# Optimization experiments

Hardware: AMD Instinct MI355X
Metric: run time of the kernel (lower is better)

## Reference

```python
import jax, jax.numpy as jnp
import numpy as np

N = 20000
E = 320000
H = 4
IN_DIM = 2000
# (in_dim, per-head out channels, concat) for each GATConv layer
LAYER_DIMS = [(2000, 128, True), (512, 64, True), (256, 32, True), (128, 64, False)]
NEG_SLOPE = 0.2  # PyG GATConv LeakyReLU slope


def setup_inputs() -> dict:
    key = jax.random.key(0)
    ks = jax.random.split(key, 2 + 4 * len(LAYER_DIMS))
    inp = {
        "x": jax.random.normal(ks[0], (N, IN_DIM), dtype=jnp.float32),
        "edge_index": jax.random.randint(ks[1], (2, E), 0, N, dtype=jnp.int64),
    }
    for i, (din, c, concat) in enumerate(LAYER_DIMS):
        k0, k1, k2, _ = jax.random.split(ks[2 + i], 4)
        inp[f"W{i}"] = (jax.random.normal(k0, (din, H * c), dtype=jnp.float32)
                         * (1.0 / np.sqrt(din)).astype(np.float32))
        inp[f"as{i}"] = jax.random.normal(k1, (H, c), dtype=jnp.float32) * 0.1
        inp[f"ad{i}"] = jax.random.normal(k2, (H, c), dtype=jnp.float32) * 0.1
        inp[f"b{i}"] = jnp.zeros((H * c if concat else c,), dtype=jnp.float32)
    return inp


def gat_conv(x, src, dst, W, att_src, att_dst, bias, concat):
    n, c = x.shape[0], W.shape[1] // H
    h = (x @ W).reshape(n, H, c)                      # (N,H,C) per-head features
    a_s = jnp.einsum("nhc,hc->nh", h, att_src)        # (N,H) source logits
    a_d = jnp.einsum("nhc,hc->nh", h, att_dst)        # (N,H) target logits
    e = a_s[src] + a_d[dst]                           # (E,H) per-edge logits
    e = jnp.where(e > 0, e, NEG_SLOPE * e)            # leaky_relu
    # segment softmax over edges sharing the same target node
    m = jax.ops.segment_max(e, dst, num_segments=n)   # (N,H)
    ex = jnp.exp(e - m[dst])
    denom = jax.ops.segment_sum(ex, dst, num_segments=n)
    alpha = ex / denom[dst]                           # (E,H)
    # weighted scatter-aggregate of source features
    out = jax.ops.segment_sum(alpha[:, :, None] * h[src], dst, num_segments=n)  # (N,H,C)
    out = out.reshape(n, H * c) if concat else out.mean(axis=1)
    return out + bias


def reference(x, edge_index, W0, as0, ad0, b0, W1, as1, ad1, b1,
              W2, as2, ad2, b2, W3, as3, ad3, b3):
    loops = jnp.arange(N, dtype=edge_index.dtype)
    src = jnp.concatenate([edge_index[0], loops])     # add self-loops (PyG default)
    dst = jnp.concatenate([edge_index[1], loops])
    params = [(W0, as0, ad0, b0), (W1, as1, ad1, b1), (W2, as2, ad2, b2), (W3, as3, ad3, b3)]
    h = x
    for i, (W, a_s, a_d, b) in enumerate(params):
        concat = LAYER_DIMS[i][2]
        h = gat_conv(h, src, dst, W, a_s, a_d, b, concat)
        if i < len(params) - 1:
            h = jax.nn.elu(h)  # dropout inactive in eval mode
    return h
```

## Files before the change

kernel.cpp:

```cpp
#include <hip/hip_runtime.h>
#include <hip/hip_bf16.h>

#define GN 20000
#define GE 320000
#define GETOT (GE + GN)
#define GH 4
#define NROW 20096

typedef __attribute__((ext_vector_type(8))) _Float16 f16x8;
typedef __attribute__((ext_vector_type(4))) float f32x4;

__global__ void detect_dtype_kernel(const void* __restrict__ ei, int* __restrict__ flag) {
    if (threadIdx.x == 0 && blockIdx.x == 0) {
        const long long* p = (const long long*)ei;
        int ok = 1;
        for (int i = 0; i < 16; ++i) {
            long long v = p[i];
            if (v < 0 || v >= GN) ok = 0;
        }
        *flag = ok;
    }
}

__device__ __forceinline__ int load_idx(const void* ei, int is64, long long pos) {
    if (is64) return (int)((const long long*)ei)[pos];
    return ((const int*)ei)[pos];
}

__global__ void hist_kernel(const void* __restrict__ ei, const int* __restrict__ flagp,
                            int* __restrict__ counts) {
    int e = blockIdx.x * blockDim.x + threadIdx.x;
    if (e >= GETOT) return;
    int d;
    if (e < GE) d = load_idx(ei, *flagp, (long long)GE + e);
    else        d = e - GE;
    atomicAdd(&counts[d], 1);
}

__global__ __launch_bounds__(1024) void scan_kernel(const int* __restrict__ counts,
                                                    int* __restrict__ offsets,
                                                    int* __restrict__ cursor) {
    __shared__ int sh[1024];
    const int tid = threadIdx.x;
    constexpr int CH = 20;
    const int base = tid * CH;
    int loc[CH];
    int sum = 0;
#pragma unroll
    for (int i = 0; i < CH; ++i) {
        int idx = base + i;
        int v = (idx < GN) ? counts[idx] : 0;
        loc[i] = sum;
        sum += v;
    }
    sh[tid] = sum;
    __syncthreads();
    for (int o = 1; o < 1024; o <<= 1) {
        int t = (tid >= o) ? sh[tid - o] : 0;
        __syncthreads();
        sh[tid] += t;
        __syncthreads();
    }
    const int excl = tid ? sh[tid - 1] : 0;
#pragma unroll
    for (int i = 0; i < CH; ++i) {
        int idx = base + i;
        if (idx < GN) {
            int o = excl + loc[i];
            offsets[idx] = o;
            cursor[idx]  = o;
        }
    }
    if (tid == 1023) offsets[GN] = sh[1023];
}

__global__ void scatter_kernel(const void* __restrict__ ei, const int* __restrict__ flagp,
                               int* __restrict__ cursor, int* __restrict__ csr_src) {
    int e = blockIdx.x * blockDim.x + threadIdx.x;
    if (e >= GETOT) return;
    int s, d;
    if (e < GE) {
        int is64 = *flagp;
        s = load_idx(ei, is64, e);
        d = load_idx(ei, is64, (long long)GE + e);
    } else {
        s = d = e - GE;
    }
    int pos = atomicAdd(&cursor[d], 1);
    csr_src[pos] = s;
}

__device__ __forceinline__ float h2f(unsigned u) {
    unsigned short us = (unsigned short)u;
    _Float16 h;
    __builtin_memcpy(&h, &us, 2);
    return (float)h;
}
__device__ __forceinline__ unsigned short f2h_bits(float v) {
    _Float16 h = (_Float16)v;
    unsigned short us;
    __builtin_memcpy(&us, &h, 2);
    return us;
}

__global__ __launch_bounds__(256) void convert_xf16(const float* __restrict__ x,
                                                    unsigned* __restrict__ xf) {
    const int CPR = 2016 / 8;
    long long idx = (long long)blockIdx.x * 256 + threadIdx.x;
    if (idx >= (long long)NROW * CPR) return;
    int row = (int)(idx / CPR);
    int col = (int)(idx % CPR) * 8;
    uint4 hp = make_uint4(0, 0, 0, 0);
    if (row < GN && col < 2000) {
        const float* p = x + (size_t)row * 2000 + col;
        float4 v0 = *(const float4*)p, v1 = *(const float4*)(p + 4);
        hp.x = (unsigned)f2h_bits(v0.x) | ((unsigned)f2h_bits(v0.y) << 16);
        hp.y = (unsigned)f2h_bits(v0.z) | ((unsigned)f2h_bits(v0.w) << 16);
        hp.z = (unsigned)f2h_bits(v1.x) | ((unsigned)f2h_bits(v1.y) << 16);
        hp.w = (unsigned)f2h_bits(v1.z) | ((unsigned)f2h_bits(v1.w) << 16);
    }
    *(uint4*)(xf + (((size_t)row * 2016 + col) >> 1)) = hp;
}

__global__ void convert_wt(const float* __restrict__ W,
                           _Float16* __restrict__ thi,
                           int K, int N, int Kpad) {
    __shared__ float tile[32][33];
    int kb = blockIdx.x * 32, nb = blockIdx.y * 32;
    for (int i = threadIdx.y; i < 32; i += 8) {
        int k = kb + i, n = nb + threadIdx.x;
        tile[i][threadIdx.x] = (k < K) ? W[(size_t)k * N + n] : 0.f;
    }
    __syncthreads();
    for (int i = threadIdx.y; i < 32; i += 8) {
        int n = nb + i, k = kb + threadIdx.x;
        thi[(size_t)n * Kpad + k] = (_Float16)tile[threadIdx.x][i];
    }
}

__device__ __forceinline__ int swz(int a) { return a ^ (((a >> 6) & 7) << 4); }
__device__ __forceinline__ int invswz(int p) {
    int b8 = (p >> 8) & 1, b7 = (p >> 7) & 1;
    int a6 = ((p >> 6) & 1) ^ b8;
    int a5 = ((p >> 5) & 1) ^ b7;
    int a4 = ((p >> 4) & 1) ^ a6;
    return (p & ~0x70) | (a4 << 4) | (a5 << 5) | (a6 << 6);
}

#define GLDS16(gsrc, ldst) __builtin_amdgcn_global_load_lds( \
    (const __attribute__((address_space(1))) void*)(gsrc),   \
    (__attribute__((address_space(3))) void*)(ldst), 16, 0, 0)

template <int MODE>
__global__ __launch_bounds__(256, 4) void gemm_f16(
        const _Float16* __restrict__ Af, int lda,
        const _Float16* __restrict__ Whi,
        int Kpad, void* __restrict__ Cp, int M, int N, int NC) {
    __shared__ char lds[32768];
    const int tid = threadIdx.x;

    const int nwg = gridDim.x;
    const int q = nwg >> 3, r = nwg & 7;
    const int xcd = blockIdx.x & 7, sub = blockIdx.x >> 3;
    const int orig = (xcd < r ? xcd * (q + 1) : r * (q + 1) + (xcd - r) * q) + sub;
    const int brow = (orig / NC) * 128;
    const int bcol = (orig % NC) * 128;

    const int lane = tid & 63, wid = tid >> 6;
    const int wr = wid >> 1, wc = wid & 1;
    const int l4 = lane & 15, kg = lane >> 4;

    int row8[2], ecol[2];
#pragma unroll
    for (int p = 0; p < 2; ++p) {
        int a = invswz(p * 4096 + tid * 16);
        row8[p] = a >> 6;
        ecol[p] = (a & 63) >> 1;
    }
    int rA[2], rB[2];
#pragma unroll
    for (int p = 0; p < 2; ++p) {
        rA[p] = brow + row8[p];
        rB[p] = bcol + row8[p];
    }

    auto STAGE = [&](int buf, int k0) {
        char* bb = lds + buf * 16384;
#pragma unroll
        for (int p = 0; p < 2; ++p) {
            GLDS16(Af  + (size_t)rA[p] * lda  + k0 + ecol[p], bb + p * 4096 + tid * 16);
            GLDS16(Whi + (size_t)rB[p] * Kpad + k0 + ecol[p], bb + 8192 + p * 4096 + tid * 16);
        }
    };

    int aoff[4], boff[4];
#pragma unroll
    for (int m = 0; m < 4; ++m) {
        aoff[m] = swz((wr * 64 + m * 16 + l4) * 64 + kg * 16);
        boff[m] = swz((wc * 64 + m * 16 + l4) * 64 + kg * 16);
    }

    f32x4 acc[4][4];
#pragma unroll
    for (int m = 0; m < 4; ++m)
#pragma unroll
        for (int n = 0; n < 4; ++n) acc[m][n] = (f32x4)(0.f);

    const int nk = Kpad / 32;
    STAGE(0, 0);

    for (int t = 0; t < nk; ++t) {
        if (t + 1 < nk) {
            STAGE((t + 1) & 1, (t + 1) * 32);
            asm volatile("s_waitcnt vmcnt(4)" ::: "memory");
        } else {
            asm volatile("s_waitcnt vmcnt(0)" ::: "memory");
        }
        __builtin_amdgcn_s_barrier();
        __builtin_amdgcn_sched_barrier(0);

        char* bb = lds + (t & 1) * 16384;
        f16x8 av[4], wh[4];
#pragma unroll
        for (int m = 0; m < 4; ++m) av[m] = *(const f16x8*)(bb + aoff[m]);
#pragma unroll
        for (int n = 0; n < 4; ++n) wh[n] = *(const f16x8*)(bb + 8192 + boff[n]);
        asm volatile("s_waitcnt lgkmcnt(0)" ::: "memory");
        __builtin_amdgcn_sched_barrier(0);

#pragma unroll
        for (int m = 0; m < 4; ++m)
#pragma unroll
            for (int n = 0; n < 4; ++n)
                acc[m][n] = __builtin_amdgcn_mfma_f32_16x16x32_f16(av[m], wh[n], acc[m][n], 0, 0, 0);
        __builtin_amdgcn_s_barrier();
    }

#pragma unroll
    for (int m = 0; m < 4; ++m) {
        int gr0 = brow + wr * 64 + m * 16 + (lane >> 4) * 4;
#pragma unroll
        for (int n = 0; n < 4; ++n) {
            int gc = bcol + wc * 64 + n * 16 + l4;
#pragma unroll
            for (int rr2 = 0; rr2 < 4; ++rr2) {
                int gr = gr0 + rr2;
                if (gr < M) {
                    size_t o = (size_t)gr * N + gc;
                    float v = acc[m][n][rr2];
                    if constexpr (MODE == 2) ((float*)Cp)[o] = v;
                    else                     ((_Float16*)Cp)[o] = (_Float16)v;
                }
            }
        }
    }
}

template <bool F16>
__global__ void att_sd_kernel(const void* __restrict__ hfeat,
                              const float* __restrict__ att_s,
                              const float* __restrict__ att_d,
                              float* __restrict__ a_s, float* __restrict__ a_d,
                              int C) {
    int wid  = (blockIdx.x * blockDim.x + threadIdx.x) >> 6;
    int lane = threadIdx.x & 63;
    if (wid >= GN) return;
#pragma unroll
    for (int h = 0; h < GH; ++h) {
        float ss = 0.f, sd = 0.f;
        for (int cc = lane; cc < C; cc += 64) {
            size_t idx = (size_t)wid * GH * C + h * C + cc;
            float v = F16 ? h2f(((const unsigned short*)hfeat)[idx])
                          : ((const float*)hfeat)[idx];
            ss += v * att_s[h * C + cc];
            sd += v * att_d[h * C + cc];
        }
#pragma unroll
        for (int o = 32; o; o >>= 1) {
            ss += __shfl_xor(ss, o);
            sd += __shfl_xor(sd, o);
        }
        if (lane == 0) { a_s[wid * GH + h] = ss; a_d[wid * GH + h] = sd; }
    }
}

template <int C, int CPT, int BLOCK>
__global__ __launch_bounds__(BLOCK) void gat_aggregate_f16(
        const unsigned short* __restrict__ hfeat,
        const float* __restrict__ a_s,
        const float* __restrict__ a_d,
        const int* __restrict__ offsets,
        const int* __restrict__ csr_src,
        const float* __restrict__ bias,
        unsigned short* __restrict__ of16) {
    constexpr int HC = GH * C;
    static_assert(BLOCK * CPT == HC, "coverage");
    const int n     = blockIdx.x;
    const int tid   = threadIdx.x;
    const int start = offsets[n];
    const int end   = offsets[n + 1];

    __shared__ float s_m[GH];
    __shared__ float s_den[GH];
    __shared__ int   s_src[64];
    __shared__ float s_al[GH][68];

    const float4 ad4 = *(const float4*)(a_d + n * GH);
    const float adh[GH] = {ad4.x, ad4.y, ad4.z, ad4.w};

    if (tid < 64) {
        float lmax[GH], lsum[GH];
#pragma unroll
        for (int h = 0; h < GH; ++h) lmax[h] = -1e30f;
        for (int e = start + tid; e < end; e += 64) {
            int s = csr_src[e];
            float4 as4 = *(const float4*)(a_s + s * GH);
            float l[GH] = {as4.x + adh[0], as4.y + adh[1], as4.z + adh[2], as4.w + adh[3]};
#pragma unroll
            for (int h = 0; h < GH; ++h) {
                float ll = l[h] > 0.f ? l[h] : 0.2f * l[h];
                lmax[h] = fmaxf(lmax[h], ll);
            }
        }
#pragma unroll
        for (int h = 0; h < GH; ++h)
#pragma unroll
            for (int o = 32; o; o >>= 1) lmax[h] = fmaxf(lmax[h], __shfl_xor(lmax[h], o));
#pragma unroll
        for (int h = 0; h < GH; ++h) lsum[h] = 0.f;
        for (int e = start + tid; e < end; e += 64) {
            int s = csr_src[e];
            float4 as4 = *(const float4*)(a_s + s * GH);
            float l[GH] = {as4.x + adh[0], as4.y + adh[1], as4.z + adh[2], as4.w + adh[3]};
#pragma unroll
            for (int h = 0; h < GH; ++h) {
                float ll = l[h] > 0.f ? l[h] : 0.2f * l[h];
                lsum[h] += __expf(ll - lmax[h]);
            }
        }
#pragma unroll
        for (int h = 0; h < GH; ++h)
#pragma unroll
            for (int o = 32; o; o >>= 1) lsum[h] += __shfl_xor(lsum[h], o);
        if (tid == 0) {
#pragma unroll
            for (int h = 0; h < GH; ++h) { s_m[h] = lmax[h]; s_den[h] = lsum[h]; }
        }
    }
    __syncthreads();

    float mm[GH], inv[GH];
#pragma unroll
    for (int h = 0; h < GH; ++h) { mm[h] = s_m[h]; inv[h] = 1.0f / s_den[h]; }

    const int ch0 = tid * CPT;
    const int hd  = ch0 / C;
    float acc[CPT];
#pragma unroll
    for (int j = 0; j < CPT; ++j) acc[j] = 0.f;

    for (int e0 = start; e0 < end; e0 += 64) {
        __syncthreads();
        if (tid < 64) {
            bool vld = (e0 + tid) < end;
            int s = vld ? csr_src[e0 + tid] : n;
            s_src[tid] = s;
            float4 as4 = *(const float4*)(a_s + s * GH);
            float l[GH] = {as4.x + adh[0], as4.y + adh[1], as4.z + adh[2], as4.w + adh[3]};
#pragma unroll
            for (int h = 0; h < GH; ++h) {
                float ll = l[h] > 0.f ? l[h] : 0.2f * l[h];
                s_al[h][tid] = vld ? __expf(ll - mm[h]) * inv[h] : 0.f;
            }
        }
        __syncthreads();
        int cnt = end - e0; if (cnt > 64) cnt = 64;
        int cnt4 = (cnt + 3) & ~3;
        for (int i = 0; i < cnt4; i += 4) {
            int4   ss = *(const int4*)&s_src[i];
            float4 aa = *(const float4*)&s_al[hd][i];
            if constexpr (CPT == 4) {
                uint2 v0 = ((const uint2*)(hfeat + (size_t)ss.x * HC))[tid];
                uint2 v1 = ((const uint2*)(hfeat + (size_t)ss.y * HC))[tid];
                uint2 v2 = ((const uint2*)(hfeat + (size_t)ss.z * HC))[tid];
                uint2 v3 = ((const uint2*)(hfeat + (size_t)ss.w * HC))[tid];
                acc[0] = fmaf(aa.x, h2f(v0.x & 0xffff), acc[0]);
                acc[1] = fmaf(aa.x, h2f(v0.x >> 16),    acc[1]);
                acc[2] = fmaf(aa.x, h2f(v0.y & 0xffff), acc[2]);
                acc[3] = fmaf(aa.x, h2f(v0.y >> 16),    acc[3]);
                acc[0] = fmaf(aa.y, h2f(v1.x & 0xffff), acc[0]);
                acc[1] = fmaf(aa.y, h2f(v1.x >> 16),    acc[1]);
                acc[2] = fmaf(aa.y, h2f(v1.y & 0xffff), acc[2]);
                acc[3] = fmaf(aa.y, h2f(v1.y >> 16),    acc[3]);
                acc[0] = fmaf(aa.z, h2f(v2.x & 0xffff), acc[0]);
                acc[1] = fmaf(aa.z, h2f(v2.x >> 16),    acc[1]);
                acc[2] = fmaf(aa.z, h2f(v2.y & 0xffff), acc[2]);
                acc[3] = fmaf(aa.z, h2f(v2.y >> 16),    acc[3]);
                acc[0] = fmaf(aa.w, h2f(v3.x & 0xffff), acc[0]);
                acc[1] = fmaf(aa.w, h2f(v3.x >> 16),    acc[1]);
                acc[2] = fmaf(aa.w, h2f(v3.y & 0xffff), acc[2]);
                acc[3] = fmaf(aa.w, h2f(v3.y >> 16),    acc[3]);
            } else {
                unsigned v0 = ((const unsigned*)(hfeat + (size_t)ss.x * HC))[tid];
                unsigned v1 = ((const unsigned*)(hfeat + (size_t)ss.y * HC))[tid];
                unsigned v2 = ((const unsigned*)(hfeat + (size_t)ss.z * HC))[tid];
                unsigned v3 = ((const unsigned*)(hfeat + (size_t)ss.w * HC))[tid];
                acc[0] = fmaf(aa.x, h2f(v0 & 0xffff), acc[0]);
                acc[1] = fmaf(aa.x, h2f(v0 >> 16),    acc[1]);
                acc[0] = fmaf(aa.y, h2f(v1 & 0xffff), acc[0]);
                acc[1] = fmaf(aa.y, h2f(v1 >> 16),    acc[1]);
                acc[0] = fmaf(aa.z, h2f(v2 & 0xffff), acc[0]);
                acc[1] = fmaf(aa.z, h2f(v2 >> 16),    acc[1]);
                acc[0] = fmaf(aa.w, h2f(v3 & 0xffff), acc[0]);
                acc[1] = fmaf(aa.w, h2f(v3 >> 16),    acc[1]);
            }
        }
    }

    unsigned short hs[CPT];
#pragma unroll
    for (int j = 0; j < CPT; ++j) {
        float v = acc[j] + bias[ch0 + j];
        v = v > 0.f ? v : expm1f(v);
        hs[j] = f2h_bits(v);
    }
    unsigned short* op = of16 + (size_t)n * HC + ch0;
    if constexpr (CPT == 4) {
        uint2 hw = make_uint2((unsigned)hs[0] | ((unsigned)hs[1] << 16),
                              (unsigned)hs[2] | ((unsigned)hs[3] << 16));
        *(uint2*)op = hw;
    } else {
        *(unsigned*)op = (unsigned)hs[0] | ((unsigned)hs[1] << 16);
    }
}

__global__ __launch_bounds__(128) void gat_aggregate_final(
        const float* __restrict__ hfeat,
        const float* __restrict__ a_s,
        const float* __restrict__ a_d,
        const int* __restrict__ offsets,
        const int* __restrict__ csr_src,
        const float* __restrict__ bias,
        float* __restrict__ outf) {
    constexpr int C = 64, HC = GH * C;
    const int n     = blockIdx.x;
    const int tid   = threadIdx.x;
    const int start = offsets[n];
    const int end   = offsets[n + 1];

    __shared__ float s_m[GH];
    __shared__ float s_den[GH];
    __shared__ int   s_src[64];
    __shared__ float s_al[GH][68];
    __shared__ float sacc[256];

    const float4 ad4 = *(const float4*)(a_d + n * GH);
    const float adh[GH] = {ad4.x, ad4.y, ad4.z, ad4.w};

    if (tid < 64) {
        float lmax[GH], lsum[GH];
#pragma unroll
        for (int h = 0; h < GH; ++h) lmax[h] = -1e30f;
        for (int e = start + tid; e < end; e += 64) {
            int s = csr_src[e];
            float4 as4 = *(const float4*)(a_s + s * GH);
            float l[GH] = {as4.x + adh[0], as4.y + adh[1], as4.z + adh[2], as4.w + adh[3]};
#pragma unroll
            for (int h = 0; h < GH; ++h) {
                float ll = l[h] > 0.f ? l[h] : 0.2f * l[h];
                lmax[h] = fmaxf(lmax[h], ll);
            }
        }
#pragma unroll
        for (int h = 0; h < GH; ++h)
#pragma unroll
            for (int o = 32; o; o >>= 1) lmax[h] = fmaxf(lmax[h], __shfl_xor(lmax[h], o));
#pragma unroll
        for (int h = 0; h < GH; ++h) lsum[h] = 0.f;
        for (int e = start + tid; e < end; e += 64) {
            int s = csr_src[e];
            float4 as4 = *(const float4*)(a_s + s * GH);
            float l[GH] = {as4.x + adh[0], as4.y + adh[1], as4.z + adh[2], as4.w + adh[3]};
#pragma unroll
            for (int h = 0; h < GH; ++h) {
                float ll = l[h] > 0.f ? l[h] : 0.2f * l[h];
                lsum[h] += __expf(ll - lmax[h]);
            }
        }
#pragma unroll
        for (int h = 0; h < GH; ++h)
#pragma unroll
            for (int o = 32; o; o >>= 1) lsum[h] += __shfl_xor(lsum[h], o);
        if (tid == 0) {
#pragma unroll
            for (int h = 0; h < GH; ++h) { s_m[h] = lmax[h]; s_den[h] = lsum[h]; }
        }
    }
    __syncthreads();

    float mm[GH], inv[GH];
#pragma unroll
    for (int h = 0; h < GH; ++h) { mm[h] = s_m[h]; inv[h] = 1.0f / s_den[h]; }

    const int hd = (2 * tid) / C;
    float2 acc = make_float2(0.f, 0.f);

    for (int e0 = start; e0 < end; e0 += 64) {
        __syncthreads();
        if (tid < 64) {
            bool vld = (e0 + tid) < end;
            int s = vld ? csr_src[e0 + tid] : n;
            s_src[tid] = s;
            float4 as4 = *(const float4*)(a_s + s * GH);
            float l[GH] = {as4.x + adh[0], as4.y + adh[1], as4.z + adh[2], as4.w + adh[3]};
#pragma unroll
            for (int h = 0; h < GH; ++h) {
                float ll = l[h] > 0.f ? l[h] : 0.2f * l[h];
                s_al[h][tid] = vld ? __expf(ll - mm[h]) * inv[h] : 0.f;
            }
        }
        __syncthreads();
        int cnt = end - e0; if (cnt > 64) cnt = 64;
        int cnt4 = (cnt + 3) & ~3;
        for (int i = 0; i < cnt4; i += 4) {
            int4   ss = *(const int4*)&s_src[i];
            float4 aa = *(const float4*)&s_al[hd][i];
            float2 v0 = ((const float2*)(hfeat + (size_t)ss.x * HC))[tid];
            float2 v1 = ((const float2*)(hfeat + (size_t)ss.y * HC))[tid];
            float2 v2 = ((const float2*)(hfeat + (size_t)ss.z * HC))[tid];
            float2 v3 = ((const float2*)(hfeat + (size_t)ss.w * HC))[tid];
            acc.x = fmaf(aa.x, v0.x, acc.x); acc.y = fmaf(aa.x, v0.y, acc.y);
            acc.x = fmaf(aa.y, v1.x, acc.x); acc.y = fmaf(aa.y, v1.y, acc.y);
            acc.x = fmaf(aa.z, v2.x, acc.x); acc.y = fmaf(aa.z, v2.y, acc.y);
            acc.x = fmaf(aa.w, v3.x, acc.x); acc.y = fmaf(aa.w, v3.y, acc.y);
        }
    }

    sacc[2 * tid]     = acc.x;
    sacc[2 * tid + 1] = acc.y;
    __syncthreads();
    if (tid < C) {
        float v = 0.f;
#pragma unroll
        for (int h = 0; h < GH; ++h) v += sacc[h * C + tid];
        outf[(size_t)n * C + tid] = v * (1.0f / GH) + bias[tid];
    }
}

extern "C" void kernel_launch(void* const* d_in, const int* in_sizes, int n_in,
                              void* d_out, int out_size, void* d_ws, size_t ws_size,
                              hipStream_t stream) {
    const float* x  = (const float*)d_in[0];
    const void*  ei = d_in[1];
    const float* W[4]  = {(const float*)d_in[2],  (const float*)d_in[6],
                          (const float*)d_in[10], (const float*)d_in[14]};
    const float* AS[4] = {(const float*)d_in[3],  (const float*)d_in[7],
                          (const float*)d_in[11], (const float*)d_in[15]};
    const float* AD[4] = {(const float*)d_in[4],  (const float*)d_in[8],
                          (const float*)d_in[12], (const float*)d_in[16]};
    const float* BI[4] = {(const float*)d_in[5],  (const float*)d_in[9],
                          (const float*)d_in[13], (const float*)d_in[17]};

    char*  w   = (char*)d_ws;
    size_t off = 0;
    auto alloc = [&](size_t b) -> char* {
        char* p = w + off;
        off += (b + 255) & ~(size_t)255;
        return p;
    };
    int*   flag    = (int*)alloc(4);
    int*   counts  = (int*)alloc((GN + 1) * sizeof(int));
    int*   offsets = (int*)alloc((GN + 1) * sizeof(int));
    int*   cursor  = (int*)alloc(GN * sizeof(int));
    int*   csr_src = (int*)alloc((size_t)GETOT * sizeof(int));
    float* a_s     = (float*)alloc((size_t)GN * GH * sizeof(float));
    float* a_d     = (float*)alloc((size_t)GN * GH * sizeof(float));
    unsigned short* hA = (unsigned short*)alloc((size_t)NROW * 512 * 2);
    unsigned short* hB = (unsigned short*)alloc((size_t)NROW * 512 * 2);
    float* hbuf    = (float*)alloc((size_t)NROW * 256 * sizeof(float));
    _Float16* wt   = (_Float16*)alloc((size_t)512 * 2016 * 2);
    _Float16* xf16 = (_Float16*)alloc((size_t)NROW * 2016 * 2);
    (void)in_sizes; (void)n_in; (void)out_size; (void)ws_size;

    detect_dtype_kernel<<<1, 64, 0, stream>>>(ei, flag);
    hipMemsetAsync(counts, 0, (GN + 1) * sizeof(int), stream);
    int eblocks = (GETOT + 255) / 256;
    hist_kernel<<<eblocks, 256, 0, stream>>>(ei, flag, counts);
    scan_kernel<<<1, 1024, 0, stream>>>(counts, offsets, cursor);
    scatter_kernel<<<eblocks, 256, 0, stream>>>(ei, flag, cursor, csr_src);

    const dim3 tb(32, 8);
    const int NR = (GN + 127) / 128;

    convert_wt<<<dim3(2016 / 32, 512 / 32), tb, 0, stream>>>(W[0], wt, 2000, 512, 2016);
    convert_xf16<<<(int)(((size_t)NROW * 252 + 255) / 256), 256, 0, stream>>>(x, (unsigned*)xf16);
    gemm_f16<0><<<NR * 4, 256, 0, stream>>>(xf16, 2016, wt, 2016, hA, GN, 512, 4);
    att_sd_kernel<true><<<(GN * 64) / 256, 256, 0, stream>>>(hA, AS[0], AD[0], a_s, a_d, 128);
    gat_aggregate_f16<128, 4, 128><<<GN, 128, 0, stream>>>(hA, a_s, a_d, offsets, csr_src,
                                                           BI[0], hB);
    convert_wt<<<dim3(512 / 32, 256 / 32), tb, 0, stream>>>(W[1], wt, 512, 256, 512);
    gemm_f16<0><<<NR * 2, 256, 0, stream>>>((_Float16*)hB, 512, wt, 512, hA, GN, 256, 2);
    att_sd_kernel<true><<<(GN * 64) / 256, 256, 0, stream>>>(hA, AS[1], AD[1], a_s, a_d, 64);
    gat_aggregate_f16<64, 4, 64><<<GN, 64, 0, stream>>>(hA, a_s, a_d, offsets, csr_src,
                                                        BI[1], hB);
    convert_wt<<<dim3(256 / 32, 128 / 32), tb, 0, stream>>>(W[2], wt, 256, 128, 256);
    gemm_f16<0><<<NR * 1, 256, 0, stream>>>((_Float16*)hB, 256, wt, 256, hA, GN, 128, 1);
    att_sd_kernel<true><<<(GN * 64) / 256, 256, 0, stream>>>(hA, AS[2], AD[2], a_s, a_d, 32);
    gat_aggregate_f16<32, 2, 64><<<GN, 64, 0, stream>>>(hA, a_s, a_d, offsets, csr_src,
                                                        BI[2], hB);
    convert_wt<<<dim3(128 / 32, 256 / 32), tb, 0, stream>>>(W[3], wt, 128, 256, 128);
    gemm_f16<2><<<NR * 2, 256, 0, stream>>>((_Float16*)hB, 128, wt, 128, hbuf, GN, 256, 2);
    att_sd_kernel<false><<<(GN * 64) / 256, 256, 0, stream>>>(hbuf, AS[3], AD[3], a_s, a_d, 64);
    gat_aggregate_final<<<GN, 128, 0, stream>>>(hbuf, a_s, a_d, offsets, csr_src,
                                                BI[3], (float*)d_out);
}
```

Before: 435.4 us.

## Fuse fp32-to-fp16 input conversion into the layer-0 GEMM with wider tiles

Drops the separate pass that converted the 20000x2000 fp32 input into a padded fp16 buffer. A new layer-0 GEMM kernel stages fp32 rows of x directly into LDS through a swizzled layout and converts them to fp16 in registers just before the MFMA. The new kernel also uses 512-thread blocks with 128x256 output tiles and 64KB of double-buffered LDS. This removes a large global write and re-read of the converted input. The cost is twice the LDS traffic for A, extra conversion instructions inside the inner loop, and possibly lower occupancy.

Result: faster. 426.0 us (-2.2%).

```diff
diff --git a/kernel.cpp b/kernel.cpp
--- a/kernel.cpp
+++ b/kernel.cpp
@@ -103,25 +103,6 @@
     return us;
 }
 
-__global__ __launch_bounds__(256) void convert_xf16(const float* __restrict__ x,
-                                                    unsigned* __restrict__ xf) {
-    const int CPR = 2016 / 8;
-    long long idx = (long long)blockIdx.x * 256 + threadIdx.x;
-    if (idx >= (long long)NROW * CPR) return;
-    int row = (int)(idx / CPR);
-    int col = (int)(idx % CPR) * 8;
-    uint4 hp = make_uint4(0, 0, 0, 0);
-    if (row < GN && col < 2000) {
-        const float* p = x + (size_t)row * 2000 + col;
-        float4 v0 = *(const float4*)p, v1 = *(const float4*)(p + 4);
-        hp.x = (unsigned)f2h_bits(v0.x) | ((unsigned)f2h_bits(v0.y) << 16);
-        hp.y = (unsigned)f2h_bits(v0.z) | ((unsigned)f2h_bits(v0.w) << 16);
-        hp.z = (unsigned)f2h_bits(v1.x) | ((unsigned)f2h_bits(v1.y) << 16);
-        hp.w = (unsigned)f2h_bits(v1.z) | ((unsigned)f2h_bits(v1.w) << 16);
-    }
-    *(uint4*)(xf + (((size_t)row * 2016 + col) >> 1)) = hp;
-}
-
 __global__ void convert_wt(const float* __restrict__ W,
                            _Float16* __restrict__ thi,
                            int K, int N, int Kpad) {
@@ -146,10 +127,132 @@
     int a4 = ((p >> 4) & 1) ^ a6;
     return (p & ~0x70) | (a4 << 4) | (a5 << 5) | (a6 << 6);
 }
+__device__ __forceinline__ int swzA32(int a) { return a ^ (((a >> 7) & 7) << 4); }
 
 #define GLDS16(gsrc, ldst) __builtin_amdgcn_global_load_lds( \
     (const __attribute__((address_space(1))) void*)(gsrc),   \
     (__attribute__((address_space(3))) void*)(ldst), 16, 0, 0)
+
+__global__ __launch_bounds__(512) void gemm_f16_l0(
+        const float* __restrict__ A32, int lda, int K,
+        const _Float16* __restrict__ Whi,
+        int Kpad, _Float16* __restrict__ Cp, int M, int N, int NC) {
+    __shared__ char lds[65536];
+    const int tid = threadIdx.x;
+
+    const int nwg = gridDim.x;
+    const int q = nwg >> 3, r = nwg & 7;
+    const int xcd = blockIdx.x & 7, sub = blockIdx.x >> 3;
+    const int orig = (xcd < r ? xcd * (q + 1) : r * (q + 1) + (xcd - r) * q) + sub;
+    const int brow = (orig / NC) * 128;
+    const int bcol = (orig % NC) * 256;
+
+    const int lane = tid & 63, wid = tid >> 6;
+    const int wr = wid >> 2, wc = wid & 3;
+    const int l4 = lane & 15, kg = lane >> 4;
+
+    int rA[2], eA[2];
+#pragma unroll
+    for (int p = 0; p < 2; ++p) {
+        int a = swzA32(p * 8192 + tid * 16);
+        int rr = brow + (a >> 7);
+        rA[p] = rr < M ? rr : M - 1;
+        eA[p] = (a & 127) >> 2;
+    }
+    int rB[2], eB[2];
+#pragma unroll
+    for (int p = 0; p < 2; ++p) {
+        int a = invswz(p * 8192 + tid * 16);
+        rB[p] = bcol + (a >> 6);
+        eB[p] = (a & 63) >> 1;
+    }
+
+    auto STAGE = [&](int buf, int k0) {
+        char* bb = lds + buf * 32768;
+#pragma unroll
+        for (int p = 0; p < 2; ++p) {
+            int kk = k0 + eA[p];
+            if (kk >= K) kk = 0;
+            GLDS16(A32 + (size_t)rA[p] * lda + kk, bb + p * 8192 + tid * 16);
+        }
+#pragma unroll
+        for (int p = 0; p < 2; ++p)
+            GLDS16(Whi + (size_t)rB[p] * Kpad + k0 + eB[p], bb + 16384 + p * 8192 + tid * 16);
+    };
+
+    int aoff[4], boff[4];
+#pragma unroll
+    for (int m = 0; m < 4; ++m) {
+        aoff[m] = swzA32((wr * 64 + m * 16 + l4) * 128 + kg * 32);
+        boff[m] = swz((wc * 64 + m * 16 + l4) * 64 + kg * 16);
+    }
+
+    f32x4 acc[4][4];
+#pragma unroll
+    for (int m = 0; m < 4; ++m)
+#pragma unroll
+        for (int n = 0; n < 4; ++n) acc[m][n] = (f32x4)(0.f);
+
+    const int nk = Kpad / 32;
+    STAGE(0, 0);
+
+    for (int t = 0; t < nk; ++t) {
+        if (t + 1 < nk) {
+            STAGE((t + 1) & 1, (t + 1) * 32);
+            asm volatile("s_waitcnt vmcnt(4)" ::: "memory");
+        } else {
+            asm volatile("s_waitcnt vmcnt(0)" ::: "memory");
+        }
+        __builtin_amdgcn_s_barrier();
+        __builtin_amdgcn_sched_barrier(0);
+
+        char* bb = lds + (t & 1) * 32768;
+        f16x8 av[4], wh[4];
+        f32x4 u0[4], u1[4];
+#pragma unroll
+        for (int m = 0; m < 4; ++m) {
+            u0[m] = *(const f32x4*)(bb + aoff[m]);
+            u1[m] = *(const f32x4*)(bb + (aoff[m] ^ 16));
+        }
+        __builtin_amdgcn_sched_barrier(0);
+#pragma unroll
+        for (int n = 0; n < 4; ++n)
+            wh[n] = *(const f16x8*)(bb + 16384 + boff[n]);
+        __builtin_amdgcn_sched_barrier(0);
+        asm volatile("s_waitcnt lgkmcnt(4)" ::: "memory");
+        __builtin_amdgcn_sched_barrier(0);
+#pragma unroll
+        for (int m = 0; m < 4; ++m) {
+            av[m][0] = (_Float16)u0[m].x; av[m][1] = (_Float16)u0[m].y;
+            av[m][2] = (_Float16)u0[m].z; av[m][3] = (_Float16)u0[m].w;
+            av[m][4] = (_Float16)u1[m].x; av[m][5] = (_Float16)u1[m].y;
+            av[m][6] = (_Float16)u1[m].z; av[m][7] = (_Float16)u1[m].w;
+        }
+        asm volatile("s_waitcnt lgkmcnt(0)" ::: "memory");
+        __builtin_amdgcn_sched_barrier(0);
+
+#pragma unroll
+        for (int m = 0; m < 4; ++m)
+#pragma unroll
+            for (int n = 0; n < 4; ++n)
+                acc[m][n] = __builtin_amdgcn_mfma_f32_16x16x32_f16(av[m], wh[n], acc[m][n], 0, 0, 0);
+        __builtin_amdgcn_s_barrier();
+    }
+
+#pragma unroll
+    for (int m = 0; m < 4; ++m) {
+        int gr0 = brow + wr * 64 + m * 16 + (lane >> 4) * 4;
+#pragma unroll
+        for (int n = 0; n < 4; ++n) {
+            int gc = bcol + wc * 64 + n * 16 + l4;
+#pragma unroll
+            for (int rr2 = 0; rr2 < 4; ++rr2) {
+                int gr = gr0 + rr2;
+                if (gr < M) Cp[(size_t)gr * N + gc] = (_Float16)acc[m][n][rr2];
+            }
+        }
+    }
+}
 
 template <int MODE>
 __global__ __launch_bounds__(256, 4) void gemm_f16(
@@ -579,7 +682,6 @@
     unsigned short* hB = (unsigned short*)alloc((size_t)NROW * 512 * 2);
     float* hbuf    = (float*)alloc((size_t)NROW * 256 * sizeof(float));
     _Float16* wt   = (_Float16*)alloc((size_t)512 * 2016 * 2);
-    _Float16* xf16 = (_Float16*)alloc((size_t)NROW * 2016 * 2);
     (void)in_sizes; (void)n_in; (void)out_size; (void)ws_size;
 
     detect_dtype_kernel<<<1, 64, 0, stream>>>(ei, flag);
@@ -593,8 +695,8 @@
     const int NR = (GN + 127) / 128;
 
     convert_wt<<<dim3(2016 / 32, 512 / 32), tb, 0, stream>>>(W[0], wt, 2000, 512, 2016);
-    convert_xf16<<<(int)(((size_t)NROW * 252 + 255) / 256), 256, 0, stream>>>(x, (unsigned*)xf16);
-    gemm_f16<0><<<NR * 4, 256, 0, stream>>>(xf16, 2016, wt, 2016, hA, GN, 512, 4);
+    gemm_f16_l0<<<NR * 2, 512, 0, stream>>>(x, 2000, 2000, wt, 2016,
+                                            (_Float16*)hA, GN, 512, 2);
     att_sd_kernel<true><<<(GN * 64) / 256, 256, 0, stream>>>(hA, AS[0], AD[0], a_s, a_d, 128);
     gat_aggregate_f16<128, 4, 128><<<GN, 128, 0, stream>>>(hA, a_s, a_d, offsets, csr_src,
                                                            BI[0], hB);
```
